# Optimization experiments

Hardware: AMD Instinct MI355X
Metric: run time of the kernel (lower is better)

The kernel has to match this reference:

```python
import math
import jax, jax.numpy as jnp
import numpy as np

B, H, N, D = 1, 16, 4096, 64
SINK_SIZE = 32
NUM_PROJS = 7
BLOCK_SIZE = 256
SAMPLE_SIZE = 256
MIN_SEQ_LEN = 1024
_SAMPLE_KEY = jax.random.key(1234)

def _hamming_perm(num_projs):
    a = np.array([0, 1])
    for _ in range(num_projs - 1):
        a = np.concatenate([a, a[::-1] + a.shape[0]])
    return jnp.asarray(a, dtype=jnp.int32)

_PERM = _hamming_perm(NUM_PROJS)
_MASK = jnp.asarray(2 ** np.arange(NUM_PROJS), dtype=jnp.int32)

def lsh_hash(x, proj_dir):
    # x: [b,h,n,d], proj_dir: [d,r] -> Gray-code-permuted bucket ids [b,h,n]
    rotated = jnp.einsum('bhnd,dr->bhnr', x, proj_dir)
    bin_ids = jnp.sum((rotated > 0).astype(jnp.int32) * _MASK, axis=-1)
    return _PERM[bin_ids]

def indexing(x, idx, chunk_size=-1):
    # gather rows along axis 2, optionally zero-pad to a multiple of chunk_size
    out = jnp.take_along_axis(x, idx[..., None], axis=2)
    if chunk_size > 0 and out.shape[2] % chunk_size != 0:
        pad = (-out.shape[2]) % chunk_size
        out = jnp.pad(out, ((0, 0), (0, 0), (0, pad), (0, 0)))
    return out

def exact_attention(q, k, v, scale, causal=False, bias=None):
    qk = jnp.einsum('bhqd,bhkd->bhqk', q, k) * scale
    if causal:
        nq, nk = q.shape[2], k.shape[2]
        cmask = jnp.triu(jnp.full((nq, nk), jnp.finfo(q.dtype).min, dtype=q.dtype), k=1)
        qk = qk + cmask
    if bias is not None:
        qk = qk + bias
    lse = jax.nn.logsumexp(qk, axis=-1, keepdims=True)
    attn = jnp.einsum('bhqk,bhkd->bhqd', jnp.exp(qk - lse), v)
    return attn, lse

def add_self_attentions(attn1, lse1, attn2, lse2):
    # attn = (attn1*e^lse1 + attn2*e^lse2)/(e^lse1+e^lse2); lse = log(e^lse1+e^lse2)
    c = jax.nn.sigmoid(lse1 - lse2)
    attn = c * attn1 + (1 - c) * attn2
    lse = jnp.logaddexp(lse1, lse2)
    return attn, lse

def forward_no_causal_mask(q, k, v, scale, proj_dir, ctr):
    b, h, nq, d = q.shape
    nk = k.shape[2]
    if MIN_SEQ_LEN > nq:
        return exact_attention(q, k, v, scale, causal=False)
    # 1) sortLSH block-diagonal attention
    q_sort_idx = jnp.argsort(lsh_hash(q, proj_dir), axis=2)  # stable
    k_sort_idx = jnp.argsort(lsh_hash(k, proj_dir), axis=2)
    q_sort_idx_inv = jnp.argsort(q_sort_idx, axis=2)
    q_sorted = indexing(q, q_sort_idx, BLOCK_SIZE)
    k_sorted = indexing(k, k_sort_idx, BLOCK_SIZE)
    v_sorted = indexing(v, k_sort_idx, BLOCK_SIZE)
    num_blocks = k_sorted.shape[2] // BLOCK_SIZE
    q_block = q_sorted.shape[2] // num_blocks
    qs = q_sorted.reshape(-1, 1, q_block, d)
    ks = k_sorted.reshape(-1, 1, BLOCK_SIZE, d)
    vs = v_sorted.reshape(-1, 1, BLOCK_SIZE, d)
    attn_block, lse_block = exact_attention(qs, ks, vs, scale, causal=False)
    attn_block = attn_block.reshape(b, h, q_sorted.shape[2], d)[:, :, :nq, :]
    lse_block = lse_block.reshape(b, h, q_sorted.shape[2], 1)[:, :, :nq, :]
    q_sorted = q_sorted[:, :, :nq, :]
    k_sorted = k_sorted[:, :, :nk, :]
    v_sorted = v_sorted[:, :, :nk, :]
    # 2) residual via uniform sampling (block-diag entries masked out)
    if SAMPLE_SIZE > 0 and nq > q_block and nk > BLOCK_SIZE:
        skey = jax.random.fold_in(_SAMPLE_KEY, ctr[0]); ctr[0] += 1
        sampled = jax.random.randint(skey, (b, h, SAMPLE_SIZE), 0, nk)
        v_sub = indexing(v_sorted, sampled)
        k_sub = indexing(k_sorted, sampled)
        q_blk_id = jnp.arange(nq) // q_block                 # [nq]
        k_blk_id = sampled // BLOCK_SIZE                     # [b,h,s]
        bias = (q_blk_id[None, None, :, None] == k_blk_id[:, :, None, :]).astype(q.dtype) * jnp.finfo(q.dtype).min
        attn_res, lse_res = exact_attention(q_sorted, k_sub, v_sub, scale, causal=False, bias=bias)
        lse_res = lse_res + math.log(nk / SAMPLE_SIZE)
        attn, lse = add_self_attentions(attn_block, lse_block, attn_res, lse_res)
    else:
        attn, lse = attn_block, lse_block
    # restore original row order
    attn = indexing(attn, q_sort_idx_inv)
    lse = indexing(lse, q_sort_idx_inv)
    return attn, lse

def hyper_causal(q, k, v, scale, proj_dir, ctr):
    b, h, n, d = q.shape
    if n <= MIN_SEQ_LEN:
        return exact_attention(q, k, v, scale, causal=True)
    n_orig = n
    if n % 2:
        q = jnp.pad(q, ((0, 0), (0, 0), (0, 1), (0, 0)))
        k = jnp.pad(k, ((0, 0), (0, 0), (0, 1), (0, 0)))
        v = jnp.pad(v, ((0, 0), (0, 0), (0, 1), (0, 0)))
    half = q.shape[2] // 2
    # recurse on the two diagonal halves (folded into head dim)
    attn_bd, lse_bd = hyper_causal(q.reshape(b, 2 * h, half, d), k.reshape(b, 2 * h, half, d), v.reshape(b, 2 * h, half, d), scale, proj_dir, ctr)
    attn_bd = attn_bd.reshape(b, h, -1, d)
    lse_bd = lse_bd.reshape(b, h, -1, 1)
    # off-diagonal lower-left block, unmasked
    attn_un, lse_un = forward_no_causal_mask(q[:, :, half:, :], k[:, :, :half, :], v[:, :, :half, :], scale, proj_dir, ctr)
    attn_up, lse_up = attn_bd[:, :, :half, :], lse_bd[:, :, :half, :]
    attn_dn, lse_dn = add_self_attentions(attn_bd[:, :, half:, :], lse_bd[:, :, half:, :], attn_un, lse_un)
    attn = jnp.concatenate([attn_up, attn_dn], axis=2)
    lse = jnp.concatenate([lse_up, lse_dn], axis=2)
    if n_orig % 2:
        attn = attn[:, :, :-1, :]
        lse = lse[:, :, :-1, :]
    return attn, lse

def _forward(query, key, value, proj_dir):
    b, h, n, d = query.shape
    scale = d ** (-0.5)
    sink = min(SINK_SIZE, n)
    prefix_attn, prefix_lse = exact_attention(query, key[:, :, :sink, :], value[:, :, :sink, :], scale, causal=True)
    if sink >= n:
        return prefix_attn
    ctr = [0]
    tail_attn, tail_lse = hyper_causal(query[:, :, sink:, :], key[:, :, sink:, :], value[:, :, sink:, :], scale, proj_dir, ctr)
    padded_tail_attn = jnp.zeros_like(prefix_attn).at[:, :, sink:, :].set(tail_attn)
    neg_inf = jnp.full_like(prefix_lse[:, :, :sink, :], jnp.finfo(prefix_lse.dtype).min)
    padded_tail_lse = jnp.concatenate([neg_inf, tail_lse], axis=2)
    attn, _ = add_self_attentions(prefix_attn, prefix_lse, padded_tail_attn, padded_tail_lse)
    return attn

def setup_inputs() -> dict:
    rng = jax.random.key(0)
    k1, k2, k3, k4 = jax.random.split(rng, 4)
    return {
        'query': jax.random.normal(k1, (B, H, N, D), jnp.float32),
        'key': jax.random.normal(k2, (B, H, N, D), jnp.float32),
        'value': jax.random.normal(k3, (B, H, N, D), jnp.float32),
        'proj_dir': jax.random.normal(k4, (D, NUM_PROJS), jnp.float32),
    }

def reference(query, key, value, proj_dir):
    return _forward(query, key, value, proj_dir)
```

## Files before the change

kernel.cpp:

```cpp
#include <hip/hip_runtime.h>
#include <hip/hip_bf16.h>
#include <math.h>
#include <stdint.h>

#define H_ 16
#define N_ 4096
#define NT_ 4064
#define NL_ 2032
#define SINK_ 32
#define SAMP_ 256
#define SCALE_ 0.125f
#define QSCALE_ 0.18033688f
#define M0L2_ 11.5415606f
#define M0_ 8.0f
#define NEGBIG_ -3.0e38f
#define LOGOFF_L2_ 2.9886841f

typedef unsigned int uint;
typedef unsigned short ushort;
typedef short bf16x8 __attribute__((ext_vector_type(8)));
typedef float f32x4 __attribute__((ext_vector_type(4)));

union B8 { uint4 u; bf16x8 b; };

__device__ __forceinline__ f32x4 mfma16(const B8& a, const B8& b, f32x4 c) {
  return __builtin_amdgcn_mfma_f32_16x16x32_bf16(a.b, b.b, c, 0, 0, 0);
}

__device__ __forceinline__ uint bfpack(float a, float b) {
  uint ua = __float_as_uint(a), ub = __float_as_uint(b);
  ua += 0x7fffu + ((ua >> 16) & 1u);
  ub += 0x7fffu + ((ub >> 16) & 1u);
  return (ua >> 16) | (ub & 0xffff0000u);
}

__device__ __forceinline__ uint cvtpk(float a, float b) {
  union { __hip_bfloat162 h; uint u; } r;
  r.h.x = __float2bfloat16(a);
  r.h.y = __float2bfloat16(b);
  return r.u;
}

__device__ __forceinline__ float bl_(uint u) { return __uint_as_float(u << 16); }
__device__ __forceinline__ float bh_(uint u) { return __uint_as_float(u & 0xffff0000u); }

__device__ __forceinline__ float logaddexpf_(float a, float b) {
  float mx = fmaxf(a, b);
  return mx + __logf(__expf(a - mx) + __expf(b - mx));
}

__device__ __forceinline__ uint32_t rotl32_(uint32_t v, uint32_t d) {
  return (v << d) | (v >> (32u - d));
}

__device__ inline void tf2x32(uint32_t k0, uint32_t k1, uint32_t& x0, uint32_t& x1) {
  uint32_t ks2 = k0 ^ k1 ^ 0x1BD11BDAu;
  x0 += k0; x1 += k1;
#define TFR(r) { x0 += x1; x1 = rotl32_(x1, r); x1 ^= x0; }
  TFR(13u) TFR(15u) TFR(26u) TFR(6u)
  x0 += k1;  x1 += ks2 + 1u;
  TFR(17u) TFR(29u) TFR(16u) TFR(24u)
  x0 += ks2; x1 += k0 + 2u;
  TFR(13u) TFR(15u) TFR(26u) TFR(6u)
  x0 += k0;  x1 += k1 + 3u;
  TFR(17u) TFR(29u) TFR(16u) TFR(24u)
  x0 += k1;  x1 += ks2 + 4u;
  TFR(13u) TFR(15u) TFR(26u) TFR(6u)
  x0 += ks2; x1 += k0 + 5u;
#undef TFR
}

__device__ __forceinline__ void nomax_sm(f32x4 s[4], float& ssum) {
#pragma unroll
  for (int st = 0; st < 4; ++st)
#pragma unroll
    for (int r = 0; r < 4; ++r) {
      s[st][r] = __builtin_exp2f(s[st][r]);
      ssum += s[st][r];
    }
}

#define PB_WRITE(SS, HK2) { \
  const f32x4 pa_ = SS[2*(HK2)], pc_ = SS[2*(HK2)+1]; \
  *(uint2*)(pw + ((((g >> 1)    ) ^ (q & 3)) * 16) + (g & 1) * 8) = \
      make_uint2(cvtpk(pa_[0], pa_[1]), cvtpk(pa_[2], pa_[3])); \
  *(uint2*)(pw + (((2 + (g >> 1)) ^ (q & 3)) * 16) + (g & 1) * 8) = \
      make_uint2(cvtpk(pc_[0], pc_[1]), cvtpk(pc_[2], pc_[3])); }
#define PB_READ(PF) { (PF).u = *(const uint4*)(pw + ((g ^ (q & 3)) * 16)); }

__device__ __forceinline__ void store_o_bf16(ushort* tp, const f32x4 o[4], float inv, int g) {
#pragma unroll
  for (int d = 0; d < 4; ++d) {
    const f32x4 r = o[d] * inv;
    *(uint2*)(tp + d * 16 + 4 * g) = make_uint2(cvtpk(r[0], r[1]), cvtpk(r[2], r[3]));
  }
}

__global__ __launch_bounds__(256) void kern_packhash(
    const float* __restrict__ K, const float* __restrict__ V, const float* __restrict__ Q,
    const float* __restrict__ proj,
    ushort* __restrict__ Kb, ushort* __restrict__ Vb, ushort* __restrict__ Vt,
    int* __restrict__ hq, int* __restrict__ hk) {
  const int bb = blockIdx.x;
  const int tid = threadIdx.x;
  if (bb < 2048) {
    const size_t idx = (size_t)bb * 256 + tid;
    const float4* s = (const float4*)(K + idx * 8);
    float4 f0 = s[0], f1 = s[1];
    uint4 p = make_uint4(bfpack(f0.x, f0.y), bfpack(f0.z, f0.w),
                         bfpack(f1.x, f1.y), bfpack(f1.z, f1.w));
    *(uint4*)(Kb + idx * 8) = p;
    return;
  }
  if (bb < 3072) {
    __shared__ ushort tr[64 * 72];
    const int u = bb - 2048;
    const int h = u >> 6, nt = u & 63;
    const int n0 = nt * 64;
    const size_t hN = (size_t)h * N_;
    const int nloc = tid >> 2, dpart = (tid & 3) * 16;
    const float4* src = (const float4*)(V + (hN + n0 + nloc) * 64 + dpart);
    float4 f0 = src[0], f1 = src[1], f2 = src[2], f3 = src[3];
    uint p0 = bfpack(f0.x, f0.y), p1 = bfpack(f0.z, f0.w);
    uint p2 = bfpack(f1.x, f1.y), p3 = bfpack(f1.z, f1.w);
    uint p4 = bfpack(f2.x, f2.y), p5 = bfpack(f2.z, f2.w);
    uint p6 = bfpack(f3.x, f3.y), p7 = bfpack(f3.z, f3.w);
    ushort* vbdst = Vb + (hN + n0 + nloc) * 64 + dpart;
    ((uint4*)vbdst)[0] = make_uint4(p0, p1, p2, p3);
    ((uint4*)vbdst)[1] = make_uint4(p4, p5, p6, p7);
    uint pv[8] = {p0, p1, p2, p3, p4, p5, p6, p7};
#pragma unroll
    for (int j = 0; j < 8; ++j) {
      tr[(dpart + 2 * j    ) * 72 + nloc] = (ushort)(pv[j] & 0xffffu);
      tr[(dpart + 2 * j + 1) * 72 + nloc] = (ushort)(pv[j] >> 16);
    }
    __syncthreads();
    const int d = tid >> 2, np = (tid & 3) * 16;
    const uint4* tp = (const uint4*)(tr + d * 72 + np);
    uint4 t0 = tp[0], t1 = tp[1];
    ushort* dst = Vt + ((size_t)(h * 64 + d)) * 4096 + n0 + np;
    ((uint4*)dst)[0] = t0;
    ((uint4*)dst)[1] = t1;
    return;
  }
  __shared__ float pr[448];
  const int u = bb - 3072;
  const int h = u & 15, tile = (u >> 4) & 7, which = u >> 7;
  for (int t = tid; t < 448; t += 256) pr[t] = proj[t];
  __syncthreads();
  const int i = tile * 256 + tid;
  if (i >= NL_) return;
  const int orig = (which == 0) ? (SINK_ + NL_ + i) : (SINK_ + i);
  const float4* x = (const float4*)((which == 0 ? Q : K) + ((size_t)h * N_ + orig) * 64);
  float xr[64];
#pragma unroll
  for (int d = 0; d < 16; ++d) {
    float4 g = x[d];
    xr[4*d+0] = g.x; xr[4*d+1] = g.y; xr[4*d+2] = g.z; xr[4*d+3] = g.w;
  }
  int bin = 0;
#pragma unroll
  for (int r = 0; r < 7; ++r) {
    float acc = 0.f;
#pragma unroll
    for (int d = 0; d < 64; ++d) acc = fmaf(xr[d], pr[d * 7 + r], acc);
    if (acc > 0.f) bin |= (1 << r);
  }
  const int g = bin ^ (bin >> 1);
  (which == 0 ? hq : hk)[h * NL_ + i] = g;
}

__global__ __launch_bounds__(256) void kern_sortsamp(
    const int* __restrict__ hq, const int* __restrict__ hk,
    int* __restrict__ q_sort, int* __restrict__ k_sort,
    int* __restrict__ samp_pos, int* __restrict__ samp_orig) {
  const int h = blockIdx.x, which = blockIdx.y;
  const int tid = threadIdx.x;

  __shared__ unsigned char keys8[NL_];
  __shared__ ushort M[64 * 130];
  __shared__ int btot[128];
  __shared__ int bscan[128];
  __shared__ ushort srt[NL_];

  const int* src = (which == 0 ? hq : hk) + h * NL_;
  for (int u = tid; u < 64 * 130 / 2; u += 256) ((uint*)M)[u] = 0u;
  for (int u = tid; u < NL_; u += 256) keys8[u] = (unsigned char)src[u];
  __syncthreads();

  if (tid < 64) {
    const int c = tid;
#pragma unroll 4
    for (int j = 0; j < 32; ++j) {
      const int u = c * 32 + j;
      if (u < NL_) ++M[c * 130 + keys8[u]];
    }
  }
  __syncthreads();

  if (tid < 128) {
    const int b = tid;
    int run = 0;
    for (int c = 0; c < 64; ++c) {
      const int v = M[c * 130 + b];
      M[c * 130 + b] = (ushort)run;
      run += v;
    }
    btot[b] = run;
    bscan[b] = run;
  }
  __syncthreads();

  for (int ofs = 1; ofs < 128; ofs <<= 1) {
    int v = 0;
    if (tid < 128 && tid >= ofs) v = bscan[tid - ofs];
    __syncthreads();
    if (tid < 128) bscan[tid] += v;
    __syncthreads();
  }

  int* dst = (which == 0 ? q_sort : k_sort) + h * NL_;
  if (tid < 64) {
    const int c = tid;
    for (int j = 0; j < 32; ++j) {
      const int u = c * 32 + j;
      if (u < NL_) {
        const int k = keys8[u];
        const int pos = (bscan[k] - btot[k]) + M[c * 130 + k];
        M[c * 130 + k] += 1;
        dst[pos] = u;
        srt[pos] = (ushort)u;
      }
    }
  }
  __syncthreads();

  if (which == 1) {
    const int s = tid;
    uint32_t a0 = 0u, a1 = 0u; tf2x32(0u, 1234u, a0, a1);
    uint32_t b0 = 0u, b1 = 0u; tf2x32(a0, a1, b0, b1);
    uint32_t c0 = 0u, c1 = 1u; tf2x32(a0, a1, c0, c1);
    const uint32_t j = (uint32_t)(h * SAMP_ + s);
    uint32_t h0 = 0u, h1 = j; tf2x32(b0, b1, h0, h1);
    uint32_t l0 = 0u, l1 = j; tf2x32(c0, c1, l0, l1);
    const uint32_t Hb = h0 ^ h1, Lb = l0 ^ l1;
    const uint32_t off = ((Hb % 2032u) * 16u + (Lb % 2032u)) % 2032u;
    samp_pos[h * SAMP_ + s] = (int)off;
    samp_orig[h * SAMP_ + s] = (int)srt[off];
  }
}

__global__ __launch_bounds__(256) void kern_attn_mfma(
    const float* __restrict__ Q, const ushort* __restrict__ Kb, const ushort* __restrict__ Vt,
    ushort* __restrict__ tailb, float* __restrict__ tail_lse,
    ushort* __restrict__ attn2b, float* __restrict__ lse2) {
  __shared__ uint kk[2304];
  __shared__ uint vv[2304];
  __shared__ uint pbuf[1024];

  const int b = blockIdx.x;
  const int tid = threadIdx.x;
  const int lane = tid & 63, w = tid >> 6;
  const int g = lane >> 4, q = lane & 15;
  const uint4 z4 = make_uint4(0, 0, 0, 0);
  const f32x4 accb = {-M0L2_, -M0L2_, -M0L2_, -M0L2_};

  int h, q0, qbase, kbase, ntiles, klen, p2slot = 0, chunkc = 0;
  bool causal;
  if (b < 512) {
    const int u = b; const int vh = u & 63;
    const int qt = 7 - (u >> 6);
    h = vh >> 2; chunkc = vh & 3;
    q0 = qt * 128;
    qbase = SINK_ + chunkc * 1016;
    kbase = qbase;
    ntiles = 2 * qt + 2; causal = true; klen = 1016;
  } else {
    const int u = b - 512; const int vh = u & 31; const int qt = (u >> 5) & 7;
    const int hf = u >> 8;
    h = vh >> 1; const int pp = vh & 1;
    q0 = qt * 128;
    qbase = SINK_ + pp * 2032 + 1016;
    kbase = SINK_ + pp * 2032 + hf * 512;
    ntiles = 8; causal = false; klen = hf ? 504 : 512;
    p2slot = hf * 32 * 1016 + vh * 1016;
  }
  const size_t hN = (size_t)h * N_;
  const int qrowA = q0 + w * 16 + q;
  const int qrowB = qrowA + 64;
  const int qcA = min(qrowA, 1015), qcB = min(qrowB, 1015);
  const int qwA_lo = q0 + w * 16, qwmaxA = qwA_lo + 15;
  const int qwB_lo = qwA_lo + 64;

  B8 qbA0, qbA1, qbB0, qbB1;
  {
    const float4* qp = (const float4*)(Q + (hN + qbase + qcA) * 64);
    float4 a = qp[2*g], c = qp[2*g+1], d = qp[8+2*g], e = qp[8+2*g+1];
    qbA0.u = make_uint4(bfpack(a.x*QSCALE_, a.y*QSCALE_), bfpack(a.z*QSCALE_, a.w*QSCALE_),
                        bfpack(c.x*QSCALE_, c.y*QSCALE_), bfpack(c.z*QSCALE_, c.w*QSCALE_));
    qbA1.u = make_uint4(bfpack(d.x*QSCALE_, d.y*QSCALE_), bfpack(d.z*QSCALE_, d.w*QSCALE_),
                        bfpack(e.x*QSCALE_, e.y*QSCALE_), bfpack(e.z*QSCALE_, e.w*QSCALE_));
    const float4* qp2 = (const float4*)(Q + (hN + qbase + qcB) * 64);
    a = qp2[2*g]; c = qp2[2*g+1]; d = qp2[8+2*g]; e = qp2[8+2*g+1];
    qbB0.u = make_uint4(bfpack(a.x*QSCALE_, a.y*QSCALE_), bfpack(a.z*QSCALE_, a.w*QSCALE_),
                        bfpack(c.x*QSCALE_, c.y*QSCALE_), bfpack(c.z*QSCALE_, c.w*QSCALE_));
    qbB1.u = make_uint4(bfpack(d.x*QSCALE_, d.y*QSCALE_), bfpack(d.z*QSCALE_, d.w*QSCALE_),
                        bfpack(e.x*QSCALE_, e.y*QSCALE_), bfpack(e.z*QSCALE_, e.w*QSCALE_));
  }
  f32x4 oA[4] = {{0,0,0,0},{0,0,0,0},{0,0,0,0},{0,0,0,0}};
  f32x4 oB[4] = {{0,0,0,0},{0,0,0,0},{0,0,0,0},{0,0,0,0}};
  float ssA = 0.f, ssB = 0.f;

  const int krow_l = tid >> 2, kpart = tid & 3;
  char* kdst = (char*)kk + krow_l * 144 + kpart * 32;
  char* vdst = (char*)vv + krow_l * 144 + kpart * 32;
  const char* kq = (const char*)kk + q * 144 + g * 16;
  const char* vq = (const char*)vv + q * 144 + g * 16;
  char* pw = (char*)pbuf + w * 1024 + q * 64;
  const size_t vtbase = ((size_t)(h * 64 + krow_l)) * 4096 + kbase + kpart * 16;

  uint4 kp0, kp1, va, va2;

#define LOADK(T) { const int kr = (T) * 64 + krow_l; \
    if (kr < klen) { const uint4* s = (const uint4*)(Kb + (hN + kbase + kr) * 64 + kpart * 16); \
      kp0 = s[0]; kp1 = s[1]; } \
    else { kp0 = z4; kp1 = z4; } }
#define LOADV(T) { const uint4* sv = (const uint4*)(Vt + vtbase + (size_t)(T) * 64); \
    va = sv[0]; va2 = sv[1]; }

  LOADK(0) LOADV(0)

  for (int t = 0; t < ntiles; ++t) {
    const int hb = t * 64;
    __syncthreads();
    *(uint4*)kdst = kp0; *(uint4*)(kdst + 16) = kp1;
    *(uint4*)vdst = va;  *(uint4*)(vdst + 16) = va2;
    __syncthreads();
    if (t + 1 < ntiles) { LOADK(t + 1) LOADV(t + 1) }

    const bool dA = !(causal && hb > qwmaxA);
    f32x4 sA[4], sB[4];
#pragma unroll
    for (int st = 0; st < 4; ++st) {
      B8 ka, kb2;
      ka.u  = *(const uint4*)(kq + (st * 16) * 144);
      kb2.u = *(const uint4*)(kq + (st * 16) * 144 + 64);
      if (dA) {
        f32x4 acc = accb;
        acc = mfma16(ka, qbA0, acc); acc = mfma16(kb2, qbA1, acc);
        sA[st] = acc;
      }
      f32x4 acc2 = accb;
      acc2 = mfma16(ka, qbB0, acc2); acc2 = mfma16(kb2, qbB1, acc2);
      sB[st] = acc2;
    }

    if (causal) {
      const int kb0 = hb + 4 * g;
      if (dA && hb + 63 > qwA_lo) {
#pragma unroll
        for (int st = 0; st < 4; ++st)
#pragma unroll
          for (int r = 0; r < 4; ++r)
            if (kb0 + st * 16 + r > qrowA) sA[st][r] = NEGBIG_;
      }
      if (hb + 63 > qwB_lo) {
#pragma unroll
        for (int st = 0; st < 4; ++st)
#pragma unroll
          for (int r = 0; r < 4; ++r)
            if (kb0 + st * 16 + r > qrowB) sB[st][r] = NEGBIG_;
      }
    } else if (hb + 63 >= klen) {
      const int kb0 = hb + 4 * g;
#pragma unroll
      for (int st = 0; st < 4; ++st)
#pragma unroll
        for (int r = 0; r < 4; ++r)
          if (kb0 + st * 16 + r >= klen) { sA[st][r] = NEGBIG_; sB[st][r] = NEGBIG_; }
    }

    if (dA) {
      nomax_sm(sA, ssA);
      nomax_sm(sB, ssB);
      __builtin_amdgcn_s_setprio(1);
#pragma unroll
      for (int hk2 = 0; hk2 < 2; ++hk2) {
        B8 pfA, pfB, vf;
        PB_WRITE(sA, hk2) PB_READ(pfA)
        PB_WRITE(sB, hk2) PB_READ(pfB)
        const int vo = hk2 * 64;
        vf.u = *(const uint4*)(vq + 0 * 2304 + vo);
        oA[0] = mfma16(vf, pfA, oA[0]); oB[0] = mfma16(vf, pfB, oB[0]);
        vf.u = *(const uint4*)(vq + 1 * 2304 + vo);
        oA[1] = mfma16(vf, pfA, oA[1]); oB[1] = mfma16(vf, pfB, oB[1]);
        vf.u = *(const uint4*)(vq + 2 * 2304 + vo);
        oA[2] = mfma16(vf, pfA, oA[2]); oB[2] = mfma16(vf, pfB, oB[2]);
        vf.u = *(const uint4*)(vq + 3 * 2304 + vo);
        oA[3] = mfma16(vf, pfA, oA[3]); oB[3] = mfma16(vf, pfB, oB[3]);
      }
      __builtin_amdgcn_s_setprio(0);
    } else {
      nomax_sm(sB, ssB);
      __builtin_amdgcn_s_setprio(1);
#pragma unroll
      for (int hk2 = 0; hk2 < 2; ++hk2) {
        B8 pfB, vf;
        PB_WRITE(sB, hk2) PB_READ(pfB)
        const int vo = hk2 * 64;
        vf.u = *(const uint4*)(vq + 0 * 2304 + vo); oB[0] = mfma16(vf, pfB, oB[0]);
        vf.u = *(const uint4*)(vq + 1 * 2304 + vo); oB[1] = mfma16(vf, pfB, oB[1]);
        vf.u = *(const uint4*)(vq + 2 * 2304 + vo); oB[2] = mfma16(vf, pfB, oB[2]);
        vf.u = *(const uint4*)(vq + 3 * 2304 + vo); oB[3] = mfma16(vf, pfB, oB[3]);
      }
      __builtin_amdgcn_s_setprio(0);
    }
  }
#undef LOADK
#undef LOADV

  ssA += __shfl_xor(ssA, 16); ssA += __shfl_xor(ssA, 32);
  ssB += __shfl_xor(ssB, 16); ssB += __shfl_xor(ssB, 32);
#pragma unroll
  for (int fr = 0; fr < 2; ++fr) {
    const int qrow = fr == 0 ? qrowA : qrowB;
    if (qrow >= 1016) continue;
    f32x4* o = fr == 0 ? oA : oB;
    const float ss = fr == 0 ? ssA : ssB;
    const float lse = M0_ + __logf(ss);
    const float inv = 1.f / ss;
    if (causal) {
      const int trow = chunkc * 1016 + qrow;
      store_o_bf16(tailb + ((size_t)h * NT_ + trow) * 64, o, inv, g);
      if (lane < 16) tail_lse[h * NT_ + trow] = lse;
    } else {
      store_o_bf16(attn2b + ((size_t)(p2slot + qrow)) * 64, o, inv, g);
      if (lane < 16) lse2[p2slot + qrow] = lse;
    }
  }
}

__global__ __launch_bounds__(256) void kern_lsh_mfma(
    const float* __restrict__ Q, const ushort* __restrict__ Kb, const ushort* __restrict__ Vb,
    const int* __restrict__ q_sort, const int* __restrict__ k_sort,
    const int* __restrict__ samp_pos, const int* __restrict__ samp_orig,
    ushort* __restrict__ attn3b, float* __restrict__ lse3) {
  __shared__ uint kk[2304];
  __shared__ uint vv[2304];
  __shared__ uint pbuf[1024];
  __shared__ float bias_s[64];

  const int b = blockIdx.x;
  const int which = b >> 8;
  const int bq = b & 255;
  const int h = bq >> 4, pt = bq & 15;
  const int tid = threadIdx.x;
  const int lane = tid & 63, w = tid >> 6;
  const int g = lane >> 4, q = lane & 15;
  const int blkq = pt >> 1;
  const size_t hN = (size_t)h * N_;

  const int pA = pt * 128 + w * 16 + q;
  const int pB = pA + 64;
  const int qiA = q_sort[h * NL_ + min(pA, NL_ - 1)];
  const int qiB = q_sort[h * NL_ + min(pB, NL_ - 1)];

  const int skey = tid >> 2, kpart = tid & 3;
  const int kpi = tid & 31, vdb = (tid >> 5) * 8;
  int kidx[4], vi0[4], vi1[4];
  float biasr[4];
#pragma unroll
  for (int t = 0; t < 4; ++t) {
    if (which == 0) {
      const int slot = blkq * 256 + t * 64 + skey;
      kidx[t] = (slot < NL_) ? k_sort[h * NL_ + slot] : -1;
      const int s0 = blkq * 256 + t * 64 + 2 * kpi;
      vi0[t] = (s0 < NL_) ? k_sort[h * NL_ + s0] : -1;
      vi1[t] = (s0 + 1 < NL_) ? k_sort[h * NL_ + s0 + 1] : -1;
    } else {
      kidx[t] = samp_orig[h * SAMP_ + t * 64 + skey];
      const int si = t * 64 + 2 * kpi;
      vi0[t] = samp_orig[h * SAMP_ + si];
      vi1[t] = samp_orig[h * SAMP_ + si + 1];
    }
  }
  if (which == 1 && tid < 64) {
#pragma unroll
    for (int j = 0; j < 4; ++j)
      biasr[j] = ((samp_pos[h * SAMP_ + j * 64 + tid] >> 8) == blkq) ? NEGBIG_ : LOGOFF_L2_;
  }

  B8 qbA0, qbA1, qbB0, qbB1;
  {
    const float4* qp = (const float4*)(Q + (hN + SINK_ + NL_ + qiA) * 64);
    float4 a = qp[2*g], c = qp[2*g+1], d = qp[8+2*g], e = qp[8+2*g+1];
    qbA0.u = make_uint4(bfpack(a.x*QSCALE_, a.y*QSCALE_), bfpack(a.z*QSCALE_, a.w*QSCALE_),
                        bfpack(c.x*QSCALE_, c.y*QSCALE_), bfpack(c.z*QSCALE_, c.w*QSCALE_));
    qbA1.u = make_uint4(bfpack(d.x*QSCALE_, d.y*QSCALE_), bfpack(d.z*QSCALE_, d.w*QSCALE_),
                        bfpack(e.x*QSCALE_, e.y*QSCALE_), bfpack(e.z*QSCALE_, e.w*QSCALE_));
    const float4* qp2 = (const float4*)(Q + (hN + SINK_ + NL_ + qiB) * 64);
    a = qp2[2*g]; c = qp2[2*g+1]; d = qp2[8+2*g]; e = qp2[8+2*g+1];
    qbB0.u = make_uint4(bfpack(a.x*QSCALE_, a.y*QSCALE_), bfpack(a.z*QSCALE_, a.w*QSCALE_),
                        bfpack(c.x*QSCALE_, c.y*QSCALE_), bfpack(c.z*QSCALE_, c.w*QSCALE_));
    qbB1.u = make_uint4(bfpack(d.x*QSCALE_, d.y*QSCALE_), bfpack(d.z*QSCALE_, d.w*QSCALE_),
                        bfpack(e.x*QSCALE_, e.y*QSCALE_), bfpack(e.z*QSCALE_, e.w*QSCALE_));
  }
  f32x4 oA[4] = {{0,0,0,0},{0,0,0,0},{0,0,0,0},{0,0,0,0}};
  f32x4 oB[4] = {{0,0,0,0},{0,0,0,0},{0,0,0,0},{0,0,0,0}};
  float ssA = 0.f, ssB = 0.f;
  const f32x4 accb = {-M0L2_, -M0L2_, -M0L2_, -M0L2_};

  char* kdst = (char*)kk + skey * 144 + kpart * 32;
  char* vdst = (char*)vv + vdb * 144 + kpi * 4;
  const char* kq = (const char*)kk + q * 144 + g * 16;
  const char* vq = (const char*)vv + q * 144 + g * 16;
  char* pw = (char*)pbuf + w * 1024 + q * 64;

  const uint4 z4 = make_uint4(0, 0, 0, 0);
  uint4 kp0, kp1, va, vb_;

#define LLOADK(T) { const int kr = kidx[T]; \
    if (kr >= 0) { const uint4* s = (const uint4*)(Kb + (hN + SINK_ + kr) * 64 + kpart * 16); \
      kp0 = s[0]; kp1 = s[1]; } else { kp0 = z4; kp1 = z4; } }
#define LLOADV(T) { const int r0 = vi0[T], r1 = vi1[T]; \
    va  = (r0 >= 0) ? *(const uint4*)(Vb + (hN + SINK_ + r0) * 64 + vdb) : z4; \
    vb_ = (r1 >= 0) ? *(const uint4*)(Vb + (hN + SINK_ + r1) * 64 + vdb) : z4; }

  LLOADK(0) LLOADV(0)

  for (int t = 0; t < 4; ++t) {
    __syncthreads();
    *(uint4*)kdst = kp0; *(uint4*)(kdst + 16) = kp1;
#define VP(JW, AW, BW) { \
    *(uint*)(vdst + (2*(JW)) * 144) = (AW & 0xffffu) | (BW << 16); \
    *(uint*)(vdst + (2*(JW) + 1) * 144) = (AW >> 16) | (BW & 0xffff0000u); }
    VP(0, va.x, vb_.x) VP(1, va.y, vb_.y) VP(2, va.z, vb_.z) VP(3, va.w, vb_.w)
#undef VP
    if (which == 1 && tid < 64) bias_s[tid] = biasr[t];
    __syncthreads();
    if (t + 1 < 4) { LLOADK(t + 1) LLOADV(t + 1) }

    f32x4 sA[4], sB[4];
#pragma unroll
    for (int st = 0; st < 4; ++st) {
      B8 ka, kb2;
      ka.u  = *(const uint4*)(kq + (st * 16) * 144);
      kb2.u = *(const uint4*)(kq + (st * 16) * 144 + 64);
      f32x4 acc = accb;
      acc = mfma16(ka, qbA0, acc); acc = mfma16(kb2, qbA1, acc);
      sA[st] = acc;
      f32x4 acc2 = accb;
      acc2 = mfma16(ka, qbB0, acc2); acc2 = mfma16(kb2, qbB1, acc2);
      sB[st] = acc2;
    }
    if (which == 1) {
      const f32x4* bp = (const f32x4*)bias_s;
#pragma unroll
      for (int st = 0; st < 4; ++st) {
        sA[st] = sA[st] + bp[st * 4 + g];
        sB[st] = sB[st] + bp[st * 4 + g];
      }
    }

    nomax_sm(sA, ssA);
    nomax_sm(sB, ssB);
    __builtin_amdgcn_s_setprio(1);
#pragma unroll
    for (int hk2 = 0; hk2 < 2; ++hk2) {
      B8 pfA, pfB, vf;
      PB_WRITE(sA, hk2) PB_READ(pfA)
      PB_WRITE(sB, hk2) PB_READ(pfB)
      const int vo = hk2 * 64;
      vf.u = *(const uint4*)(vq + 0 * 2304 + vo);
      oA[0] = mfma16(vf, pfA, oA[0]); oB[0] = mfma16(vf, pfB, oB[0]);
      vf.u = *(const uint4*)(vq + 1 * 2304 + vo);
      oA[1] = mfma16(vf, pfA, oA[1]); oB[1] = mfma16(vf, pfB, oB[1]);
      vf.u = *(const uint4*)(vq + 2 * 2304 + vo);
      oA[2] = mfma16(vf, pfA, oA[2]); oB[2] = mfma16(vf, pfB, oB[2]);
      vf.u = *(const uint4*)(vq + 3 * 2304 + vo);
      oA[3] = mfma16(vf, pfA, oA[3]); oB[3] = mfma16(vf, pfB, oB[3]);
    }
    __builtin_amdgcn_s_setprio(0);
  }
#undef LLOADK
#undef LLOADV

  ssA += __shfl_xor(ssA, 16); ssA += __shfl_xor(ssA, 32);
  ssB += __shfl_xor(ssB, 16); ssB += __shfl_xor(ssB, 32);
  const size_t obase = (size_t)which * 16 * NL_;
#pragma unroll
  for (int fr = 0; fr < 2; ++fr) {
    const int p = fr == 0 ? pA : pB;
    if (p >= NL_) continue;
    const int qi = fr == 0 ? qiA : qiB;
    f32x4* o = fr == 0 ? oA : oB;
    const float ss = fr == 0 ? ssA : ssB;
    const float un = M0_ + __logf(ss);
    const float inv = 1.f / ss;
    store_o_bf16(attn3b + (obase + (size_t)h * NL_ + qi) * 64, o, inv, g);
    if (lane < 16) lse3[obase + h * NL_ + qi] = un;
  }
}

__global__ __launch_bounds__(128) void kern_final(
    const float* __restrict__ Q, const float* __restrict__ K, const float* __restrict__ V,
    const ushort* __restrict__ tailb, const float* __restrict__ tail_lse,
    const ushort* __restrict__ attn2b, const float* __restrict__ lse2,
    const ushort* __restrict__ attn3b, const float* __restrict__ lse3,
    float* __restrict__ out) {
  const int h = blockIdx.x;
  const int r = blockIdx.y * 128 + (int)threadIdx.x;

  __shared__ float4 kk[SINK_ * 16];
  __shared__ float4 vv[SINK_ * 16];
  for (int u = threadIdx.x; u < SINK_ * 16; u += 128) {
    const int row = u >> 4, d4 = u & 15;
    kk[u] = ((const float4*)(K + ((size_t)h * N_ + row) * 64))[d4];
    vv[u] = ((const float4*)(V + ((size_t)h * N_ + row) * 64))[d4];
  }
  __syncthreads();

  float4 q4[16], acc[16];
  const float4* qp = (const float4*)(Q + ((size_t)h * N_ + r) * 64);
#pragma unroll
  for (int d = 0; d < 16; ++d) { q4[d] = qp[d]; acc[d] = make_float4(0.f, 0.f, 0.f, 0.f); }

  float ssum = 0.f;
  const int nk = min(SINK_, r + 1);
  for (int j = 0; j < nk; ++j) {
    float s = 0.f;
#pragma unroll
    for (int d = 0; d < 16; ++d) {
      float4 x = q4[d], y = kk[j * 16 + d];
      s = fmaf(x.x, y.x, s); s = fmaf(x.y, y.y, s);
      s = fmaf(x.z, y.z, s); s = fmaf(x.w, y.w, s);
    }
    const float wgt = __expf(fmaf(s, SCALE_, -M0_));
    ssum += wgt;
    const float4* v4 = &vv[j * 16];
#pragma unroll
    for (int d = 0; d < 16; ++d) {
      acc[d].x = fmaf(wgt, v4[d].x, acc[d].x);
      acc[d].y = fmaf(wgt, v4[d].y, acc[d].y);
      acc[d].z = fmaf(wgt, v4[d].z, acc[d].z);
      acc[d].w = fmaf(wgt, v4[d].w, acc[d].w);
    }
  }
  const float pl = M0_ + __logf(ssum);
  const float inv = 1.f / ssum;
  float4* op = (float4*)(out + ((size_t)h * N_ + r) * 64);
  if (r < SINK_) {
#pragma unroll
    for (int d = 0; d < 16; ++d)
      op[d] = make_float4(acc[d].x * inv, acc[d].y * inv, acc[d].z * inv, acc[d].w * inv);
    return;
  }

  const int t = r - SINK_;
  float a[64];
  {
    const uint4* tp = (const uint4*)(tailb + ((size_t)h * NT_ + t) * 64);
#pragma unroll
    for (int j = 0; j < 8; ++j) {
      const uint4 u = tp[j];
      a[8*j+0] = bl_(u.x); a[8*j+1] = bh_(u.x);
      a[8*j+2] = bl_(u.y); a[8*j+3] = bh_(u.y);
      a[8*j+4] = bl_(u.z); a[8*j+5] = bh_(u.z);
      a[8*j+6] = bl_(u.w); a[8*j+7] = bh_(u.w);
    }
  }
  float al = tail_lse[h * NT_ + t];

  const int pp = (t >= NL_) ? 1 : 0;
  const int tloc = t - pp * NL_;
  if (tloc >= 1016) {
    const int vh = h * 2 + pp, i = tloc - 1016;
    const float l20 = lse2[vh * 1016 + i];
    const float l21 = lse2[32 * 1016 + vh * 1016 + i];
    const float c12 = 1.f / (1.f + __expf(l21 - l20));
    const float l2 = logaddexpf_(l20, l21);
    const float c = 1.f / (1.f + __expf(l2 - al));
    const uint4* b0 = (const uint4*)(attn2b + ((size_t)(vh * 1016 + i)) * 64);
    const uint4* b1 = (const uint4*)(attn2b + ((size_t)(32 * 1016 + vh * 1016 + i)) * 64);
#pragma unroll
    for (int j = 0; j < 8; ++j) {
      const uint4 u0 = b0[j], u1 = b1[j];
      float x0[8] = {bl_(u0.x), bh_(u0.x), bl_(u0.y), bh_(u0.y), bl_(u0.z), bh_(u0.z), bl_(u0.w), bh_(u0.w)};
      float x1[8] = {bl_(u1.x), bh_(u1.x), bl_(u1.y), bh_(u1.y), bl_(u1.z), bh_(u1.z), bl_(u1.w), bh_(u1.w)};
#pragma unroll
      for (int e = 0; e < 8; ++e) {
        const float bb = c12 * x0[e] + (1.f - c12) * x1[e];
        a[8*j+e] = c * a[8*j+e] + (1.f - c) * bb;
      }
    }
    al = logaddexpf_(al, l2);
  }
  if (t >= NL_) {
    const int qi = t - NL_;
    const float l3a = lse3[h * NL_ + qi];
    const float l3b = lse3[16 * NL_ + h * NL_ + qi];
    const float c34 = 1.f / (1.f + __expf(l3b - l3a));
    const float l3 = logaddexpf_(l3a, l3b);
    const float c = 1.f / (1.f + __expf(l3 - al));
    const uint4* b0 = (const uint4*)(attn3b + ((size_t)(h * NL_ + qi)) * 64);
    const uint4* b1 = (const uint4*)(attn3b + ((size_t)(16 * NL_ + h * NL_ + qi)) * 64);
#pragma unroll
    for (int j = 0; j < 8; ++j) {
      const uint4 u0 = b0[j], u1 = b1[j];
      float x0[8] = {bl_(u0.x), bh_(u0.x), bl_(u0.y), bh_(u0.y), bl_(u0.z), bh_(u0.z), bl_(u0.w), bh_(u0.w)};
      float x1[8] = {bl_(u1.x), bh_(u1.x), bl_(u1.y), bh_(u1.y), bl_(u1.z), bh_(u1.z), bl_(u1.w), bh_(u1.w)};
#pragma unroll
      for (int e = 0; e < 8; ++e) {
        const float bb = c34 * x0[e] + (1.f - c34) * x1[e];
        a[8*j+e] = c * a[8*j+e] + (1.f - c) * bb;
      }
    }
    al = logaddexpf_(al, l3);
  }
  const float cc = 1.f / (1.f + __expf(al - pl));
#pragma unroll
  for (int d = 0; d < 16; ++d)
    op[d] = make_float4(cc * acc[d].x * inv + (1.f - cc) * a[4*d+0],
                        cc * acc[d].y * inv + (1.f - cc) * a[4*d+1],
                        cc * acc[d].z * inv + (1.f - cc) * a[4*d+2],
                        cc * acc[d].w * inv + (1.f - cc) * a[4*d+3]);
}

extern "C" void kernel_launch(void* const* d_in, const int* in_sizes, int n_in,
                              void* d_out, int out_size, void* d_ws, size_t ws_size,
                              hipStream_t stream) {
  (void)in_sizes; (void)n_in; (void)out_size; (void)ws_size;
  const float* Q = (const float*)d_in[0];
  const float* K = (const float*)d_in[1];
  const float* V = (const float*)d_in[2];
  const float* proj = (const float*)d_in[3];
  float* out = (float*)d_out;

  char* w = (char*)d_ws;
  auto carve = [&](size_t bytes) { char* p = w; w += (bytes + 255) & ~(size_t)255; return p; };
  ushort* tailb  = (ushort*)carve((size_t)H_ * NT_ * 64 * sizeof(ushort));
  float* tail_lse = (float*)carve((size_t)H_ * NT_ * sizeof(float));
  ushort* attn2b = (ushort*)carve((size_t)2 * 32 * 1016 * 64 * sizeof(ushort));
  float* lse2    = (float*)carve((size_t)2 * 32 * 1016 * sizeof(float));
  ushort* attn3b = (ushort*)carve((size_t)2 * H_ * NL_ * 64 * sizeof(ushort));
  float* lse3    = (float*)carve((size_t)2 * H_ * NL_ * sizeof(float));
  ushort* Kb     = (ushort*)carve((size_t)H_ * N_ * 64 * sizeof(ushort));
  ushort* Vb     = (ushort*)carve((size_t)H_ * N_ * 64 * sizeof(ushort));
  ushort* Vt     = (ushort*)carve((size_t)H_ * N_ * 64 * sizeof(ushort) + 4096);
  int* hq        = (int*)carve((size_t)H_ * NL_ * sizeof(int));
  int* hk        = (int*)carve((size_t)H_ * NL_ * sizeof(int));
  int* q_sort    = (int*)carve((size_t)H_ * NL_ * sizeof(int));
  int* k_sort    = (int*)carve((size_t)H_ * NL_ * sizeof(int));
  int* samp_pos  = (int*)carve((size_t)H_ * SAMP_ * sizeof(int));
  int* samp_orig = (int*)carve((size_t)H_ * SAMP_ * sizeof(int));

  kern_packhash<<<dim3(3328), 256, 0, stream>>>(K, V, Q, proj, Kb, Vb, Vt, hq, hk);
  kern_sortsamp<<<dim3(H_, 2), 256, 0, stream>>>(hq, hk, q_sort, k_sort, samp_pos, samp_orig);
  kern_attn_mfma<<<dim3(1024), 256, 0, stream>>>(Q, Kb, Vt, tailb, tail_lse, attn2b, lse2);
  kern_lsh_mfma<<<dim3(512), 256, 0, stream>>>(Q, Kb, Vb, q_sort, k_sort, samp_pos, samp_orig,
                                               attn3b, lse3);
  kern_final<<<dim3(H_, 32), 128, 0, stream>>>(Q, K, V, tailb, tail_lse,
                                               attn2b, lse2, attn3b, lse3, out);
}
```

Baseline: 127.9 us.

## Split long causal diagonal tiles into two key halves merged in final kernel

Causal query tiles in the upper half of each 1016-row chunk are split into two work items: one attends keys 0-511 without masking and another attends keys 512+ causally, written to a new attn4/lse4 buffer. The final kernel merges the extra partial result with logsumexp weighting. This shortens the longest workgroups and balances load across the grid, reordering launches so heavy blocks start first. In exchange it adds 256 extra blocks, a new intermediate buffer and extra reads and blending in the final pass.

Measured after the change: 130.2 us. Within noise of the previous version (+1.7%).

```diff
diff --git a/kernel.cpp b/kernel.cpp
--- a/kernel.cpp
+++ b/kernel.cpp
@@ -253,7 +253,8 @@
 __global__ __launch_bounds__(256) void kern_attn_mfma(
     const float* __restrict__ Q, const ushort* __restrict__ Kb, const ushort* __restrict__ Vt,
     ushort* __restrict__ tailb, float* __restrict__ tail_lse,
-    ushort* __restrict__ attn2b, float* __restrict__ lse2) {
+    ushort* __restrict__ attn2b, float* __restrict__ lse2,
+    ushort* __restrict__ attn4b, float* __restrict__ lse4) {
   __shared__ uint kk[2304];
   __shared__ uint vv[2304];
   __shared__ uint pbuf[1024];
@@ -265,18 +266,10 @@
   const uint4 z4 = make_uint4(0, 0, 0, 0);
   const f32x4 accb = {-M0L2_, -M0L2_, -M0L2_, -M0L2_};
 
-  int h, q0, qbase, kbase, ntiles, klen, p2slot = 0, chunkc = 0;
+  int h, q0, qbase, kbase, ntiles, klen, koff = 0, p2slot = 0, chunkc = 0, outmode;
   bool causal;
   if (b < 512) {
-    const int u = b; const int vh = u & 63;
-    const int qt = 7 - (u >> 6);
-    h = vh >> 2; chunkc = vh & 3;
-    q0 = qt * 128;
-    qbase = SINK_ + chunkc * 1016;
-    kbase = qbase;
-    ntiles = 2 * qt + 2; causal = true; klen = 1016;
-  } else {
-    const int u = b - 512; const int vh = u & 31; const int qt = (u >> 5) & 7;
+    const int u = b; const int vh = u & 31; const int qt = (u >> 5) & 7;
     const int hf = u >> 8;
     h = vh >> 1; const int pp = vh & 1;
     q0 = qt * 128;
@@ -284,12 +277,41 @@
     kbase = SINK_ + pp * 2032 + hf * 512;
     ntiles = 8; causal = false; klen = hf ? 504 : 512;
     p2slot = hf * 32 * 1016 + vh * 1016;
+    outmode = 1;
+  } else if (b < 768) {
+    const int u = b - 512; const int vh = u & 63;
+    const int qt = 4 + (u >> 6);
+    h = vh >> 2; chunkc = vh & 3;
+    q0 = qt * 128;
+    qbase = SINK_ + chunkc * 1016;
+    kbase = qbase;
+    ntiles = 8; causal = false; klen = 512;
+    outmode = 0;
+  } else if (b < 1024) {
+    const int u = b - 768; const int vh = u & 63;
+    const int qt = 7 - (u >> 6);
+    h = vh >> 2; chunkc = vh & 3;
+    q0 = qt * 128;
+    qbase = SINK_ + chunkc * 1016;
+    kbase = qbase + 512;
+    ntiles = 2 * (qt - 4) + 2; causal = true; klen = 504; koff = 512;
+    outmode = 2;
+  } else {
+    const int u = b - 1024; const int vh = u & 63;
+    const int qt = 3 - (u >> 6);
+    h = vh >> 2; chunkc = vh & 3;
+    q0 = qt * 128;
+    qbase = SINK_ + chunkc * 1016;
+    kbase = qbase;
+    ntiles = 2 * qt + 2; causal = true; klen = 1016;
+    outmode = 0;
   }
   const size_t hN = (size_t)h * N_;
   const int qrowA = q0 + w * 16 + q;
   const int qrowB = qrowA + 64;
   const int qcA = min(qrowA, 1015), qcB = min(qrowB, 1015);
-  const int qwA_lo = q0 + w * 16, qwmaxA = qwA_lo + 15;
+  const int qeA = qrowA - koff, qeB = qrowB - koff;
+  const int qwA_lo = q0 + w * 16 - koff, qwmaxA = qwA_lo + 15;
   const int qwB_lo = qwA_lo + 64;
 
   B8 qbA0, qbA1, qbB0, qbB1;
@@ -362,14 +384,14 @@
         for (int st = 0; st < 4; ++st)
 #pragma unroll
           for (int r = 0; r < 4; ++r)
-            if (kb0 + st * 16 + r > qrowA) sA[st][r] = NEGBIG_;
+            if (kb0 + st * 16 + r > qeA) sA[st][r] = NEGBIG_;
       }
       if (hb + 63 > qwB_lo) {
 #pragma unroll
         for (int st = 0; st < 4; ++st)
 #pragma unroll
           for (int r = 0; r < 4; ++r)
-            if (kb0 + st * 16 + r > qrowB) sB[st][r] = NEGBIG_;
+            if (kb0 + st * 16 + r > qeB) sB[st][r] = NEGBIG_;
       }
     } else if (hb + 63 >= klen) {
       const int kb0 = hb + 4 * g;
@@ -429,14 +451,22 @@
     const float ss = fr == 0 ? ssA : ssB;
     const float lse = M0_ + __logf(ss);
     const float inv = 1.f / ss;
-    if (causal) {
+    ushort* tp;
+    float* lp;
+    if (outmode == 0) {
       const int trow = chunkc * 1016 + qrow;
-      store_o_bf16(tailb + ((size_t)h * NT_ + trow) * 64, o, inv, g);
-      if (lane < 16) tail_lse[h * NT_ + trow] = lse;
+      tp = tailb + ((size_t)h * NT_ + trow) * 64;
+      lp = tail_lse + h * NT_ + trow;
+    } else if (outmode == 1) {
+      tp = attn2b + ((size_t)(p2slot + qrow)) * 64;
+      lp = lse2 + p2slot + qrow;
     } else {
-      store_o_bf16(attn2b + ((size_t)(p2slot + qrow)) * 64, o, inv, g);
-      if (lane < 16) lse2[p2slot + qrow] = lse;
-    }
+      const int trow = chunkc * 1016 + qrow;
+      tp = attn4b + ((size_t)h * NT_ + trow) * 64;
+      lp = lse4 + h * NT_ + trow;
+    }
+    store_o_bf16(tp, o, inv, g);
+    if (lane < 16) *lp = lse;
   }
 }
 
@@ -607,6 +637,7 @@
     const ushort* __restrict__ tailb, const float* __restrict__ tail_lse,
     const ushort* __restrict__ attn2b, const float* __restrict__ lse2,
     const ushort* __restrict__ attn3b, const float* __restrict__ lse3,
+    const ushort* __restrict__ attn4b, const float* __restrict__ lse4,
     float* __restrict__ out) {
   const int h = blockIdx.x;
   const int r = blockIdx.y * 128 + (int)threadIdx.x;
@@ -670,6 +701,23 @@
     }
   }
   float al = tail_lse[h * NT_ + t];
+
+  const int chunk = t / 1016;
+  const int qrow = t - chunk * 1016;
+  if (qrow >= 512) {
+    const float l4 = lse4[h * NT_ + t];
+    const float c = 1.f / (1.f + __expf(l4 - al));
+    const uint4* bp = (const uint4*)(attn4b + ((size_t)h * NT_ + t) * 64);
+#pragma unroll
+    for (int j = 0; j < 8; ++j) {
+      const uint4 u1 = bp[j];
+      float x1[8] = {bl_(u1.x), bh_(u1.x), bl_(u1.y), bh_(u1.y), bl_(u1.z), bh_(u1.z), bl_(u1.w), bh_(u1.w)};
+#pragma unroll
+      for (int e = 0; e < 8; ++e)
+        a[8*j+e] = c * a[8*j+e] + (1.f - c) * x1[e];
+    }
+    al = logaddexpf_(al, l4);
+  }
 
   const int pp = (t >= NL_) ? 1 : 0;
   const int tloc = t - pp * NL_;
@@ -744,6 +792,8 @@
   float* lse2    = (float*)carve((size_t)2 * 32 * 1016 * sizeof(float));
   ushort* attn3b = (ushort*)carve((size_t)2 * H_ * NL_ * 64 * sizeof(ushort));
   float* lse3    = (float*)carve((size_t)2 * H_ * NL_ * sizeof(float));
+  ushort* attn4b = (ushort*)carve((size_t)H_ * NT_ * 64 * sizeof(ushort));
+  float* lse4    = (float*)carve((size_t)H_ * NT_ * sizeof(float));
   ushort* Kb     = (ushort*)carve((size_t)H_ * N_ * 64 * sizeof(ushort));
   ushort* Vb     = (ushort*)carve((size_t)H_ * N_ * 64 * sizeof(ushort));
   ushort* Vt     = (ushort*)carve((size_t)H_ * N_ * 64 * sizeof(ushort) + 4096);
@@ -756,9 +806,10 @@
 
   kern_packhash<<<dim3(3328), 256, 0, stream>>>(K, V, Q, proj, Kb, Vb, Vt, hq, hk);
   kern_sortsamp<<<dim3(H_, 2), 256, 0, stream>>>(hq, hk, q_sort, k_sort, samp_pos, samp_orig);
-  kern_attn_mfma<<<dim3(1024), 256, 0, stream>>>(Q, Kb, Vt, tailb, tail_lse, attn2b, lse2);
+  kern_attn_mfma<<<dim3(1280), 256, 0, stream>>>(Q, Kb, Vt, tailb, tail_lse,
+                                                 attn2b, lse2, attn4b, lse4);
   kern_lsh_mfma<<<dim3(512), 256, 0, stream>>>(Q, Kb, Vb, q_sort, k_sort, samp_pos, samp_orig,
                                                attn3b, lse3);
   kern_final<<<dim3(H_, 32), 128, 0, stream>>>(Q, K, V, tailb, tail_lse,
-                                               attn2b, lse2, attn3b, lse3, out);
-}
+                                               attn2b, lse2, attn3b, lse3, attn4b, lse4, out);
+}
```
